# Optimization experiments

Hardware: AMD Instinct MI355X
Metric: run time of the kernel (lower is better)

Reference implementation:

```python
import jax, jax.numpy as jnp
import numpy as np

B, C_IN, L = 4, 512, 16384
C_RED = C_IN // 2  # q/k/v reduced channels = 256
BL = 64            # sliding-window block size
NEG = -jnp.inf


def setup_inputs() -> dict:
    key = jax.random.key(0)
    ks = jax.random.split(key, 8)
    x1 = jax.random.normal(ks[0], (B, C_IN, L), dtype=jnp.float32)
    x2 = jax.random.normal(ks[1], (B, C_IN, L), dtype=jnp.float32)
    mask = jnp.ones((B, 1, L), dtype=jnp.float32)
    s = 0.02
    Wq = jax.random.normal(ks[2], (C_RED, C_IN), dtype=jnp.float32) * s
    Wk = jax.random.normal(ks[3], (C_RED, C_IN), dtype=jnp.float32) * s
    Wv = jax.random.normal(ks[4], (C_RED, C_IN), dtype=jnp.float32) * s
    Wo = jax.random.normal(ks[5], (C_IN, C_RED), dtype=jnp.float32) * s
    bq = jnp.zeros((C_RED,), jnp.float32)
    bk = jnp.zeros((C_RED,), jnp.float32)
    bv = jnp.zeros((C_RED,), jnp.float32)
    bo = jnp.zeros((C_IN,), jnp.float32)
    return {"x1": x1, "x2": x2, "mask": mask, "Wq": Wq, "bq": bq,
            "Wk": Wk, "bk": bk, "Wv": Wv, "bv": bv, "Wo": Wo, "bo": bo}


def _conv1x1(W, b, x):
    # x: (B, Cin, L) -> (B, Cout, L)
    return jnp.einsum('oc,bcl->bol', W, x) + b[None, :, None]


def reference(x1, x2, mask, Wq, bq, Wk, bk, Wv, bv, Wo, bo):
    # encoder stage: value comes from x1 (x2 unused)
    q = _conv1x1(Wq, bq, x1)  # (B, C, L)
    k = _conv1x1(Wk, bk, x1)
    v = _conv1x1(Wv, bv, x1)

    Bq, C, Lq = q.shape
    bl = BL
    nb = (Lq + bl - 1) // bl
    pad = nb * bl - Lq
    if pad > 0:
        q = jnp.pad(q, ((0, 0), (0, 0), (0, pad)))
        k = jnp.pad(k, ((0, 0), (0, 0), (0, pad)))
        v = jnp.pad(v, ((0, 0), (0, 0), (0, pad)))
        mask = jnp.pad(mask, ((0, 0), (0, 0), (0, pad)))

    # non-overlapping windows: (B, C, nb, bl)
    qb = q.reshape(Bq, C, nb, bl)
    kb = k.reshape(Bq, C, nb, bl)
    vb = v.reshape(Bq, C, nb, bl)
    mb = mask.reshape(Bq, 1, nb, bl)  # (B,1,nb,bl)

    scale = 1.0 / jnp.sqrt(jnp.float32(C))
    # per-block attention scores: (B, nb, bl_i, bl_j)
    scores = jnp.einsum('bcni,bcnj->bnij', qb, kb) * scale
    key_mask = mb[:, 0, :, None, :]  # (B, nb, 1, bl_j)
    scores = jnp.where(key_mask == 0, NEG, scores)
    probs = jax.nn.softmax(scores, axis=-1)
    attn = jnp.einsum('bnij,bcnj->bcni', probs, vb)  # (B, C, nb, bl)

    h = jax.nn.relu(attn)
    out = jnp.einsum('oc,bcni->boni', Wo, h) + bo[None, :, None, None]
    out = out.reshape(Bq, Wo.shape[0], nb * bl)
    if pad > 0:
        out = out[:, :, :Lq]
    return out
```

## Files before the change

kernel.cpp:

```cpp
#include <hip/hip_runtime.h>
#include <hip/hip_fp16.h>
#include <stdint.h>

#define BB    4
#define CIN   512
#define CRED  256
#define LL    16384
#define NBLK  256
#define WELEM 131072

typedef _Float16 half8 __attribute__((ext_vector_type(8)));
typedef float    f32x4 __attribute__((ext_vector_type(4)));

#define XT_OFF 0
#define Q_OFF  0
#define K_OFF  32768
#define V_OFF  32768
#define H_OFF  0
#define P_OFF  65536
#define MSK_OFF 73728
#define LDS_BYTES 73984

#define SWZ(r) (((r)&7)<<4)

__global__ void convert_weights(const float* __restrict__ Wq,
                                const float* __restrict__ Wk,
                                const float* __restrict__ Wv,
                                const float* __restrict__ Wo,
                                _Float16* __restrict__ dst) {
    int i = blockIdx.x * blockDim.x + threadIdx.x;
    int m = i >> 17;
    int e = i & (WELEM - 1);
    const float* src = (m == 0) ? Wq : (m == 1) ? Wk : (m == 2) ? Wv : Wo;
    dst[(size_t)m * WELEM + e] = (_Float16)src[e];
}

__global__ __launch_bounds__(512, 4)
void att_fused(const float* __restrict__ x1, const float* __restrict__ mask,
               const _Float16* __restrict__ W,
               const float* __restrict__ bq, const float* __restrict__ bk,
               const float* __restrict__ bv, const float* __restrict__ bo,
               float* __restrict__ out) {
    extern __shared__ char lds[];
    const int tid  = threadIdx.x;
    const int wid  = tid >> 6;
    const int lane = tid & 63;
    const int l15  = lane & 15;
    const int l4   = lane >> 4;
    const int blk  = blockIdx.x;
    const int b    = blk >> 8;
    const int n    = blk & 255;

    const _Float16* Wq = W;
    const _Float16* Wk = W + WELEM;
    const _Float16* Wv = W + 2 * WELEM;
    const _Float16* Wo = W + 3 * WELEM;

    {
        const int jx = tid & 15;
        const int rb = tid >> 4;
        const float* r0 = x1 + ((size_t)b * CIN + 2 * rb) * LL + n * 64 + 4 * jx;
        #pragma unroll
        for (int i = 0; i < 8; ++i) {
            f32x4 a = *(const f32x4*)(r0 + (size_t)(64 * i) * LL);
            f32x4 c = *(const f32x4*)(r0 + (size_t)(64 * i + 1) * LL);
            const int col = 4 * rb + 128 * i;
            #pragma unroll
            for (int u = 0; u < 4; ++u) {
                union { _Float16 h[2]; uint32_t w; } p;
                p.h[0] = (_Float16)a[u];
                p.h[1] = (_Float16)c[u];
                const int j = 4 * jx + u;
                *(uint32_t*)(lds + XT_OFF + j * 1024 + (col ^ SWZ(j))) = p.w;
            }
        }
        if (tid < 64)
            *(float*)(lds + MSK_OFF + tid * 4) = mask[(size_t)b * LL + n * 64 + tid];
    }
    __syncthreads();

    uint64_t qh[2][4], kh[2][4], vh[2][4];
    {
        #pragma unroll
        for (int pass = 0; pass < 2; ++pass) {
            f32x4 aQ[4], aK[4], aV[4];
            #pragma unroll
            for (int q = 0; q < 4; ++q) {
                aQ[q] = (f32x4){0.f, 0.f, 0.f, 0.f};
                aK[q] = (f32x4){0.f, 0.f, 0.f, 0.f};
                aV[q] = (f32x4){0.f, 0.f, 0.f, 0.f};
            }
            const int mrow = wid * 32 + pass * 16 + l15;
            const _Float16* wqp = Wq + (size_t)mrow * CIN + l4 * 8;
            const _Float16* wkp = Wk + (size_t)mrow * CIN + l4 * 8;
            const _Float16* wvp = Wv + (size_t)mrow * CIN + l4 * 8;
            #pragma unroll 4
            for (int ks = 0; ks < 16; ++ks) {
                const int kb = ks * 64 + l4 * 16;
                half8 xb[4];
                #pragma unroll
                for (int nt = 0; nt < 4; ++nt) {
                    const int j = nt * 16 + l15;
                    xb[nt] = *(const half8*)(lds + XT_OFF + j * 1024 + (kb ^ SWZ(j)));
                }
                half8 aq = *(const half8*)(wqp + ks * 32);
                half8 ak = *(const half8*)(wkp + ks * 32);
                half8 av = *(const half8*)(wvp + ks * 32);
                #pragma unroll
                for (int nt = 0; nt < 4; ++nt) {
                    aQ[nt] = __builtin_amdgcn_mfma_f32_16x16x32_f16(aq, xb[nt], aQ[nt], 0, 0, 0);
                    aK[nt] = __builtin_amdgcn_mfma_f32_16x16x32_f16(ak, xb[nt], aK[nt], 0, 0, 0);
                    aV[nt] = __builtin_amdgcn_mfma_f32_16x16x32_f16(av, xb[nt], aV[nt], 0, 0, 0);
                }
            }
            const int c0 = wid * 32 + pass * 16 + l4 * 4;
            f32x4 bqv = *(const f32x4*)(bq + c0);
            f32x4 bkv = *(const f32x4*)(bk + c0);
            f32x4 bvv = *(const f32x4*)(bv + c0);
            #pragma unroll
            for (int nt = 0; nt < 4; ++nt) {
                union { _Float16 h[4]; uint64_t q; } qp, kp, vp;
                #pragma unroll
                for (int ri = 0; ri < 4; ++ri) {
                    qp.h[ri] = (_Float16)(aQ[nt][ri] + bqv[ri]);
                    kp.h[ri] = (_Float16)(aK[nt][ri] + bkv[ri]);
                    vp.h[ri] = (_Float16)(aV[nt][ri] + bvv[ri]);
                }
                qh[pass][nt] = qp.q;
                kh[pass][nt] = kp.q;
                vh[pass][nt] = vp.q;
            }
        }
    }
    __syncthreads();

    #pragma unroll
    for (int pass = 0; pass < 2; ++pass) {
        const int c0 = wid * 32 + pass * 16 + l4 * 4;
        #pragma unroll
        for (int nt = 0; nt < 4; ++nt) {
            const int j = nt * 16 + l15;
            *(uint64_t*)(lds + Q_OFF + j * 512 + ((2 * c0) ^ SWZ(j))) = qh[pass][nt];
            *(uint64_t*)(lds + K_OFF + j * 512 + ((2 * c0) ^ SWZ(j))) = kh[pass][nt];
        }
    }
    __syncthreads();

    if (wid < 4) {
        const int i0 = wid * 16;
        f32x4 sa[4];
        #pragma unroll
        for (int jt = 0; jt < 4; ++jt) sa[jt] = (f32x4){0.f, 0.f, 0.f, 0.f};
        #pragma unroll
        for (int ks = 0; ks < 8; ++ks) {
            const int kb = ks * 64 + l4 * 16;
            const int iq = i0 + l15;
            half8 qa = *(const half8*)(lds + Q_OFF + iq * 512 + (kb ^ SWZ(iq)));
            #pragma unroll
            for (int jt = 0; jt < 4; ++jt) {
                const int jr = jt * 16 + l15;
                half8 kf = *(const half8*)(lds + K_OFF + jr * 512 + (kb ^ SWZ(jr)));
                sa[jt] = __builtin_amdgcn_mfma_f32_16x16x32_f16(qa, kf, sa[jt], 0, 0, 0);
            }
        }
        float msk[4];
        #pragma unroll
        for (int jt = 0; jt < 4; ++jt)
            msk[jt] = *(const float*)(lds + MSK_OFF + (jt * 16 + l15) * 4);
        #pragma unroll
        for (int ri = 0; ri < 4; ++ri) {
            float v[4];
            #pragma unroll
            for (int jt = 0; jt < 4; ++jt)
                v[jt] = (msk[jt] == 0.f) ? -1e30f : sa[jt][ri] * 0.0625f;
            float mx = fmaxf(fmaxf(v[0], v[1]), fmaxf(v[2], v[3]));
            mx = fmaxf(mx, __shfl_xor(mx, 1));
            mx = fmaxf(mx, __shfl_xor(mx, 2));
            mx = fmaxf(mx, __shfl_xor(mx, 4));
            mx = fmaxf(mx, __shfl_xor(mx, 8));
            float e[4], sum = 0.f;
            #pragma unroll
            for (int jt = 0; jt < 4; ++jt) { e[jt] = __expf(v[jt] - mx); sum += e[jt]; }
            sum += __shfl_xor(sum, 1);
            sum += __shfl_xor(sum, 2);
            sum += __shfl_xor(sum, 4);
            sum += __shfl_xor(sum, 8);
            const float inv = 1.f / sum;
            const int i = i0 + l4 * 4 + ri;
            #pragma unroll
            for (int jt = 0; jt < 4; ++jt) {
                const int j = jt * 16 + l15;
                *(_Float16*)(lds + P_OFF + i * 128 + ((2 * j) ^ SWZ(i))) =
                    (_Float16)(e[jt] * inv);
            }
        }
    }
    __syncthreads();

    #pragma unroll
    for (int pass = 0; pass < 2; ++pass) {
        const int c0 = wid * 32 + pass * 16 + l4 * 4;
        #pragma unroll
        for (int nt = 0; nt < 4; ++nt) {
            const int j = nt * 16 + l15;
            const uint64_t v64 = vh[pass][nt];
            #pragma unroll
            for (int ri = 0; ri < 4; ++ri) {
                const int c = c0 + ri;
                *(uint16_t*)(lds + V_OFF + c * 128 + ((2 * j) ^ SWZ(c))) =
                    (uint16_t)(v64 >> (16 * ri));
            }
        }
    }
    __syncthreads();

    {
        const int cb = wid * 32;
        f32x4 pv[2][4];
        #pragma unroll
        for (int m = 0; m < 2; ++m)
            #pragma unroll
            for (int q = 0; q < 4; ++q) pv[m][q] = (f32x4){0.f, 0.f, 0.f, 0.f};
        #pragma unroll
        for (int ks = 0; ks < 2; ++ks) {
            const int kb = ks * 64 + l4 * 16;
            half8 pb[4];
            #pragma unroll
            for (int nt = 0; nt < 4; ++nt) {
                const int i = nt * 16 + l15;
                pb[nt] = *(const half8*)(lds + P_OFF + i * 128 + (kb ^ SWZ(i)));
            }
            #pragma unroll
            for (int mt = 0; mt < 2; ++mt) {
                const int c = cb + mt * 16 + l15;
                half8 va = *(const half8*)(lds + V_OFF + c * 128 + (kb ^ SWZ(c)));
                #pragma unroll
                for (int nt = 0; nt < 4; ++nt)
                    pv[mt][nt] = __builtin_amdgcn_mfma_f32_16x16x32_f16(va, pb[nt], pv[mt][nt], 0, 0, 0);
            }
        }
        #pragma unroll
        for (int mt = 0; mt < 2; ++mt) {
            const int c0 = cb + mt * 16 + l4 * 4;
            #pragma unroll
            for (int nt = 0; nt < 4; ++nt) {
                const int j = nt * 16 + l15;
                union { _Float16 h[4]; uint64_t q; } hp;
                #pragma unroll
                for (int ri = 0; ri < 4; ++ri)
                    hp.h[ri] = (_Float16)fmaxf(pv[mt][nt][ri], 0.f);
                *(uint64_t*)(lds + H_OFF + j * 512 + ((2 * c0) ^ SWZ(j))) = hp.q;
            }
        }
    }
    __syncthreads();

    {
        const int mbo = wid * 64;
        const _Float16* wob = Wo + (size_t)(mbo + l15) * CRED + l4 * 8;
        f32x4 oa[4][4];
        #pragma unroll
        for (int m = 0; m < 4; ++m)
            #pragma unroll
            for (int q = 0; q < 4; ++q) oa[m][q] = (f32x4){0.f, 0.f, 0.f, 0.f};
        #pragma unroll 4
        for (int ks = 0; ks < 8; ++ks) {
            const int kb = ks * 64 + l4 * 16;
            half8 hb[4];
            #pragma unroll
            for (int nt = 0; nt < 4; ++nt) {
                const int i = nt * 16 + l15;
                hb[nt] = *(const half8*)(lds + H_OFF + i * 512 + (kb ^ SWZ(i)));
            }
            #pragma unroll
            for (int mt = 0; mt < 4; ++mt) {
                half8 wa = *(const half8*)(wob + mt * 16 * CRED + ks * 32);
                #pragma unroll
                for (int nt = 0; nt < 4; ++nt)
                    oa[mt][nt] = __builtin_amdgcn_mfma_f32_16x16x32_f16(wa, hb[nt], oa[mt][nt], 0, 0, 0);
            }
        }
        #pragma unroll
        for (int mt = 0; mt < 4; ++mt) {
            const int o0 = mbo + mt * 16 + l4 * 4;
            f32x4 bov = *(const f32x4*)(bo + o0);
            #pragma unroll
            for (int ri = 0; ri < 4; ++ri) {
                float* orow = out + ((size_t)b * CIN + (o0 + ri)) * LL + n * 64;
                #pragma unroll
                for (int nt = 0; nt < 4; ++nt)
                    orow[nt * 16 + l15] = oa[mt][nt][ri] + bov[ri];
            }
        }
    }
}

extern "C" void kernel_launch(void* const* d_in, const int* in_sizes, int n_in,
                              void* d_out, int out_size, void* d_ws, size_t ws_size,
                              hipStream_t stream) {
    const float* x1   = (const float*)d_in[0];
    const float* mask = (const float*)d_in[2];
    const float* Wq   = (const float*)d_in[3];
    const float* bq   = (const float*)d_in[4];
    const float* Wk   = (const float*)d_in[5];
    const float* bk   = (const float*)d_in[6];
    const float* Wv   = (const float*)d_in[7];
    const float* bv   = (const float*)d_in[8];
    const float* Wo   = (const float*)d_in[9];
    const float* bo   = (const float*)d_in[10];
    float* out = (float*)d_out;
    _Float16* wbuf = (_Float16*)d_ws;

    (void)hipFuncSetAttribute((const void*)att_fused,
                              hipFuncAttributeMaxDynamicSharedMemorySize, LDS_BYTES);

    convert_weights<<<2048, 256, 0, stream>>>(Wq, Wk, Wv, Wo, wbuf);
    att_fused<<<BB * NBLK, 512, LDS_BYTES, stream>>>(x1, mask, wbuf, bq, bk, bv, bo, out);
}
```

Measured before the change: 174.1 us.

## Defer V projection until after softmax, reloading x1 to cut live registers

The V projection is split out of the fused QKV GEMM and run after the score/softmax stage. Because the x-transpose buffer in LDS gets overwritten by Q/K, x1 is reloaded from global memory into registers before the score stage and rewritten to LDS before the V GEMM. This shortens the live range of the V accumulators and may lower register pressure or raise occupancy. In exchange it reads x1 twice from global memory, holds 64 extra float registers across the softmax, and adds two more barriers.

```diff
diff --git a/kernel.cpp b/kernel.cpp
--- a/kernel.cpp
+++ b/kernel.cpp
@@ -50,20 +50,21 @@
     const int blk  = blockIdx.x;
     const int b    = blk >> 8;
     const int n    = blk & 255;
+    const int jx   = tid & 15;
+    const int rb   = tid >> 4;
 
     const _Float16* Wq = W;
     const _Float16* Wk = W + WELEM;
     const _Float16* Wv = W + 2 * WELEM;
     const _Float16* Wo = W + 3 * WELEM;
 
+    const float* xbase = x1 + ((size_t)b * CIN + 2 * rb) * LL + n * 64 + 4 * jx;
+
     {
-        const int jx = tid & 15;
-        const int rb = tid >> 4;
-        const float* r0 = x1 + ((size_t)b * CIN + 2 * rb) * LL + n * 64 + 4 * jx;
         #pragma unroll
         for (int i = 0; i < 8; ++i) {
-            f32x4 a = *(const f32x4*)(r0 + (size_t)(64 * i) * LL);
-            f32x4 c = *(const f32x4*)(r0 + (size_t)(64 * i + 1) * LL);
+            f32x4 a = *(const f32x4*)(xbase + (size_t)(64 * i) * LL);
+            f32x4 c = *(const f32x4*)(xbase + (size_t)(64 * i + 1) * LL);
             const int col = 4 * rb + 128 * i;
             #pragma unroll
             for (int u = 0; u < 4; ++u) {
@@ -79,57 +80,48 @@
     }
     __syncthreads();
 
-    uint64_t qh[2][4], kh[2][4], vh[2][4];
-    {
-        #pragma unroll
-        for (int pass = 0; pass < 2; ++pass) {
-            f32x4 aQ[4], aK[4], aV[4];
-            #pragma unroll
-            for (int q = 0; q < 4; ++q) {
-                aQ[q] = (f32x4){0.f, 0.f, 0.f, 0.f};
-                aK[q] = (f32x4){0.f, 0.f, 0.f, 0.f};
-                aV[q] = (f32x4){0.f, 0.f, 0.f, 0.f};
-            }
-            const int mrow = wid * 32 + pass * 16 + l15;
-            const _Float16* wqp = Wq + (size_t)mrow * CIN + l4 * 8;
-            const _Float16* wkp = Wk + (size_t)mrow * CIN + l4 * 8;
-            const _Float16* wvp = Wv + (size_t)mrow * CIN + l4 * 8;
-            #pragma unroll 4
-            for (int ks = 0; ks < 16; ++ks) {
-                const int kb = ks * 64 + l4 * 16;
-                half8 xb[4];
-                #pragma unroll
-                for (int nt = 0; nt < 4; ++nt) {
-                    const int j = nt * 16 + l15;
-                    xb[nt] = *(const half8*)(lds + XT_OFF + j * 1024 + (kb ^ SWZ(j)));
-                }
-                half8 aq = *(const half8*)(wqp + ks * 32);
-                half8 ak = *(const half8*)(wkp + ks * 32);
-                half8 av = *(const half8*)(wvp + ks * 32);
-                #pragma unroll
-                for (int nt = 0; nt < 4; ++nt) {
-                    aQ[nt] = __builtin_amdgcn_mfma_f32_16x16x32_f16(aq, xb[nt], aQ[nt], 0, 0, 0);
-                    aK[nt] = __builtin_amdgcn_mfma_f32_16x16x32_f16(ak, xb[nt], aK[nt], 0, 0, 0);
-                    aV[nt] = __builtin_amdgcn_mfma_f32_16x16x32_f16(av, xb[nt], aV[nt], 0, 0, 0);
-                }
-            }
-            const int c0 = wid * 32 + pass * 16 + l4 * 4;
-            f32x4 bqv = *(const f32x4*)(bq + c0);
-            f32x4 bkv = *(const f32x4*)(bk + c0);
-            f32x4 bvv = *(const f32x4*)(bv + c0);
-            #pragma unroll
-            for (int nt = 0; nt < 4; ++nt) {
-                union { _Float16 h[4]; uint64_t q; } qp, kp, vp;
-                #pragma unroll
-                for (int ri = 0; ri < 4; ++ri) {
-                    qp.h[ri] = (_Float16)(aQ[nt][ri] + bqv[ri]);
-                    kp.h[ri] = (_Float16)(aK[nt][ri] + bkv[ri]);
-                    vp.h[ri] = (_Float16)(aV[nt][ri] + bvv[ri]);
-                }
-                qh[pass][nt] = qp.q;
-                kh[pass][nt] = kp.q;
-                vh[pass][nt] = vp.q;
-            }
+    uint64_t qh[2][4], kh[2][4];
+    #pragma unroll
+    for (int pass = 0; pass < 2; ++pass) {
+        f32x4 aQ[4], aK[4];
+        #pragma unroll
+        for (int q = 0; q < 4; ++q) {
+            aQ[q] = (f32x4){0.f, 0.f, 0.f, 0.f};
+            aK[q] = (f32x4){0.f, 0.f, 0.f, 0.f};
+        }
+        const int mrow = wid * 32 + pass * 16 + l15;
+        const _Float16* wqp = Wq + (size_t)mrow * CIN + l4 * 8;
+        const _Float16* wkp = Wk + (size_t)mrow * CIN + l4 * 8;
+        #pragma unroll 4
+        for (int ks = 0; ks < 16; ++ks) {
+            const int kb = ks * 64 + l4 * 16;
+            half8 xb[4];
+            #pragma unroll
+            for (int nt = 0; nt < 4; ++nt) {
+                const int j = nt * 16 + l15;
+                xb[nt] = *(const half8*)(lds + XT_OFF + j * 1024 + (kb ^ SWZ(j)));
+            }
+            half8 aq = *(const half8*)(wqp + ks * 32);
+            half8 ak = *(const half8*)(wkp + ks * 32);
+            #pragma unroll
+            for (int nt = 0; nt < 4; ++nt) {
+                aQ[nt] = __builtin_amdgcn_mfma_f32_16x16x32_f16(aq, xb[nt], aQ[nt], 0, 0, 0);
+                aK[nt] = __builtin_amdgcn_mfma_f32_16x16x32_f16(ak, xb[nt], aK[nt], 0, 0, 0);
+            }
+        }
+        const int c0 = wid * 32 + pass * 16 + l4 * 4;
+        f32x4 bqv = *(const f32x4*)(bq + c0);
+        f32x4 bkv = *(const f32x4*)(bk + c0);
+        #pragma unroll
+        for (int nt = 0; nt < 4; ++nt) {
+            union { _Float16 h[4]; uint64_t q; } qp, kp;
+            #pragma unroll
+            for (int ri = 0; ri < 4; ++ri) {
+                qp.h[ri] = (_Float16)(aQ[nt][ri] + bqv[ri]);
+                kp.h[ri] = (_Float16)(aK[nt][ri] + bkv[ri]);
+            }
+            qh[pass][nt] = qp.q;
+            kh[pass][nt] = kp.q;
         }
     }
     __syncthreads();
@@ -145,6 +137,13 @@
         }
     }
     __syncthreads();
+
+    f32x4 rE[8], rO[8];
+    #pragma unroll
+    for (int i = 0; i < 8; ++i) {
+        rE[i] = *(const f32x4*)(xbase + (size_t)(64 * i) * LL);
+        rO[i] = *(const f32x4*)(xbase + (size_t)(64 * i + 1) * LL);
+    }
 
     if (wid < 4) {
         const int i0 = wid * 16;
@@ -198,12 +197,67 @@
     __syncthreads();
 
     #pragma unroll
-    for (int pass = 0; pass < 2; ++pass) {
-        const int c0 = wid * 32 + pass * 16 + l4 * 4;
+    for (int i = 0; i < 8; ++i) {
+        const int col = 4 * rb + 128 * i;
+        #pragma unroll
+        for (int u = 0; u < 4; ++u) {
+            union { _Float16 h[2]; uint32_t w; } p;
+            p.h[0] = (_Float16)rE[i][u];
+            p.h[1] = (_Float16)rO[i][u];
+            const int j = 4 * jx + u;
+            *(uint32_t*)(lds + XT_OFF + j * 1024 + (col ^ SWZ(j))) = p.w;
+        }
+    }
+    __syncthreads();
+
+    uint64_t vh[2][4];
+    {
+        f32x4 aV[2][4];
+        #pragma unroll
+        for (int m = 0; m < 2; ++m)
+            #pragma unroll
+            for (int q = 0; q < 4; ++q) aV[m][q] = (f32x4){0.f, 0.f, 0.f, 0.f};
+        const _Float16* wvp = Wv + (size_t)(wid * 32 + l15) * CIN + l4 * 8;
+        #pragma unroll 4
+        for (int ks = 0; ks < 16; ++ks) {
+            const int kb = ks * 64 + l4 * 16;
+            half8 xb[4];
+            #pragma unroll
+            for (int nt = 0; nt < 4; ++nt) {
+                const int j = nt * 16 + l15;
+                xb[nt] = *(const half8*)(lds + XT_OFF + j * 1024 + (kb ^ SWZ(j)));
+            }
+            #pragma unroll
+            for (int mt = 0; mt < 2; ++mt) {
+                half8 av = *(const half8*)(wvp + mt * 16 * CIN + ks * 32);
+                #pragma unroll
+                for (int nt = 0; nt < 4; ++nt)
+                    aV[mt][nt] = __builtin_amdgcn_mfma_f32_16x16x32_f16(av, xb[nt], aV[mt][nt], 0, 0, 0);
+            }
+        }
+        #pragma unroll
+        for (int mt = 0; mt < 2; ++mt) {
+            const int c0 = wid * 32 + mt * 16 + l4 * 4;
+            f32x4 bvv = *(const f32x4*)(bv + c0);
+            #pragma unroll
+            for (int nt = 0; nt < 4; ++nt) {
+                union { _Float16 h[4]; uint64_t q; } vp;
+                #pragma unroll
+                for (int ri = 0; ri < 4; ++ri)
+                    vp.h[ri] = (_Float16)(aV[mt][nt][ri] + bvv[ri]);
+                vh[mt][nt] = vp.q;
+            }
+        }
+    }
+    __syncthreads();
+
+    #pragma unroll
+    for (int mt = 0; mt < 2; ++mt) {
+        const int c0 = wid * 32 + mt * 16 + l4 * 4;
         #pragma unroll
         for (int nt = 0; nt < 4; ++nt) {
             const int j = nt * 16 + l15;
-            const uint64_t v64 = vh[pass][nt];
+            const uint64_t v64 = vh[mt][nt];
             #pragma unroll
             for (int ri = 0; ri < 4; ++ri) {
                 const int c = c0 + ri;
```

Result: slower. 209.6 us (+20.4%).
